# Kernel tuning notes

Hardware: AMD Instinct MI355X
Metric: run time of the kernel (lower is better)

The kernel has to match this reference:

```python
import jax, jax.numpy as jnp
import numpy as np
from jax import lax

B, N, NPOINT, NSAMPLE = 8, 8192, 2048, 32
RADIUS = 0.2
D_FEAT = 64
MLP = [64, 64, 128]
IN_CH = 3 + D_FEAT
EPS = 1e-5


def setup_inputs() -> dict:
    key = jax.random.key(0)
    ks = jax.random.split(key, 2 + len(MLP))
    inp = {
        "xyz": jax.random.uniform(ks[0], (B, N, 3), dtype=jnp.float32),
        "points": jax.random.normal(ks[1], (B, N, D_FEAT), dtype=jnp.float32),
    }
    cin = IN_CH
    for i, cout in enumerate(MLP):
        inp[f"W{i+1}"] = jax.random.normal(ks[2 + i], (cout, cin), dtype=jnp.float32) * 0.05
        inp[f"b{i+1}"] = jnp.zeros((cout,), jnp.float32)
        inp[f"g{i+1}"] = jnp.ones((cout,), jnp.float32)
        inp[f"be{i+1}"] = jnp.zeros((cout,), jnp.float32)
        cin = cout
    return inp


def farthest_point_sample(xyz, npoint):
    # xyz: (B, N, 3) -> (B, npoint) int32 indices. Deterministic start at index 0.
    Bb, Nn, _ = xyz.shape
    barange = jnp.arange(Bb)

    def step(carry, _):
        distance, farthest = carry
        centroid = xyz[barange, farthest]                      # (B, 3)
        d = jnp.sum((xyz - centroid[:, None, :]) ** 2, -1)     # (B, N)
        distance = jnp.minimum(distance, d)
        new_far = jnp.argmax(distance, axis=-1).astype(jnp.int32)
        return (distance, new_far), farthest

    init = (jnp.full((Bb, Nn), 1e10, xyz.dtype), jnp.zeros((Bb,), jnp.int32))
    _, idxs = lax.scan(step, init, None, length=npoint)        # (npoint, B)
    return idxs.T                                              # (B, npoint)


def index_points(points, idx):
    # points: (B, N, C); idx: (B, S) or (B, S, K)
    return jax.vmap(lambda p, i: p[i])(points, idx)


def square_distance(src, dst):
    # (B, S, C) x (B, N, C) -> (B, S, N)
    d = -2.0 * jnp.einsum('bsc,bnc->bsn', src, dst)
    d += jnp.sum(src ** 2, -1)[:, :, None]
    d += jnp.sum(dst ** 2, -1)[:, None, :]
    return d


def query_ball_point(radius, nsample, xyz, new_xyz):
    Bb, Nn, _ = xyz.shape
    sqr = square_distance(new_xyz, xyz)                        # (B, S, N)
    grid = jnp.arange(Nn, dtype=jnp.int32)
    group_idx = jnp.where(sqr > radius * radius, Nn, grid)     # invalid -> N
    # nsample smallest indices == torch sort(dim=-1)[:, :, :nsample]
    neg_vals, _ = lax.top_k(-group_idx, nsample)               # (B, S, K)
    group_idx = -neg_vals
    first = group_idx[:, :, 0:1]
    return jnp.where(group_idx == Nn, first, group_idx)


def bn_relu(x, gamma, beta):
    # x: (B, C, L). Training-mode batchnorm (biased variance) + ReLU.
    mean = jnp.mean(x, axis=(0, 2), keepdims=True)
    var = jnp.mean((x - mean) ** 2, axis=(0, 2), keepdims=True)
    xn = (x - mean) * lax.rsqrt(var + EPS)
    return jax.nn.relu(xn * gamma[None, :, None] + beta[None, :, None])


def reference(xyz, points, W1, b1, g1, be1, W2, b2, g2, be2, W3, b3, g3, be3):
    Bb = xyz.shape[0]
    fps_idx = farthest_point_sample(xyz, NPOINT)               # (B, S)
    new_xyz = index_points(xyz, fps_idx)                       # (B, S, 3)
    idx = query_ball_point(RADIUS, NSAMPLE, xyz, new_xyz)      # (B, S, K)
    grouped_xyz = index_points(xyz, idx)                       # (B, S, K, 3)
    grouped_xyz_norm = grouped_xyz - new_xyz[:, :, None, :]
    grouped_points = index_points(points, idx)                 # (B, S, K, D)
    g = jnp.concatenate([grouped_xyz_norm, grouped_points], -1)  # (B, S, K, C)
    x = g.reshape(Bb, NPOINT * NSAMPLE, -1).transpose(0, 2, 1)   # (B, C, S*K)
    for W, b, ga, be in ((W1, b1, g1, be1), (W2, b2, g2, be2), (W3, b3, g3, be3)):
        x = jnp.einsum('oc,bcl->bol', W, x) + b[None, :, None]
        x = bn_relu(x, ga, be)
    x = x.reshape(Bb, -1, NPOINT, NSAMPLE)
    new_points = jnp.max(x, axis=-1).transpose(0, 2, 1)        # (B, S, C_out)
    return new_xyz, new_points
```

## Files before the change

### kernel.cpp

```cpp
#include <hip/hip_runtime.h>
#include <hip/hip_bf16.h>

#define NB 8
#define NN 8192
#define NP 2048
#define NS 32
#define INV_P (1.0f/524288.0f)

typedef float v2f __attribute__((ext_vector_type(2)));

template<int CTRL>
__device__ __forceinline__ float fmax_dpp(float v) {
  const int x = __builtin_amdgcn_update_dpp(0, __float_as_int(v), CTRL, 0xF, 0xF, true);
  return fmaxf(v, __int_as_float(x));
}


__global__ __launch_bounds__(512)
void k_fps_pre(const float* __restrict__ xyz, const float* __restrict__ feat,
               const float* __restrict__ W1, const float* __restrict__ b1,
               float* __restrict__ F, float* __restrict__ outXyz, float* __restrict__ stats)
{
#pragma clang fp contract(off)
  __shared__ union U { float4 xyzw[NN]; float fx[128*64]; } sh;
  __shared__ unsigned long long cand[2][8];
  const int t = threadIdx.x;
  if (blockIdx.x < 8) {
    const int b = blockIdx.x;
    const float* xb = xyz + (size_t)b*NN*3;
    v2f px[8], py[8], pz[8], dd[8];
#pragma unroll
    for (int j = 0; j < 8; ++j) {
      const int i0 = t*16 + 2*j;
      const float x0 = xb[i0*3+0], y0 = xb[i0*3+1], z0 = xb[i0*3+2];
      const float x1 = xb[i0*3+3], y1 = xb[i0*3+4], z1 = xb[i0*3+5];
      px[j] = (v2f){x0,x1}; py[j] = (v2f){y0,y1}; pz[j] = (v2f){z0,z1};
      dd[j] = (v2f){1e10f,1e10f};
      sh.xyzw[i0]   = make_float4(x0,y0,z0,0.f);
      sh.xyzw[i0+1] = make_float4(x1,y1,z1,0.f);
    }
    __syncthreads();
    const int lane = t & 63, wv = t >> 6;
    float4 cf = sh.xyzw[0];
    for (int s = 0; s < NP; ++s) {
      if (t == 0) {
        float* o = outXyz + ((size_t)b*NP+s)*3;
        o[0]=cf.x; o[1]=cf.y; o[2]=cf.z;
      }
      const v2f cx = {cf.x,cf.x}, cy = {cf.y,cf.y}, cz = {cf.z,cf.z};
      float m = -1.f; int mi = 0;
#pragma unroll
      for (int j = 0; j < 8; ++j) {
        const v2f dx = px[j]-cx, dy = py[j]-cy, dz = pz[j]-cz;
        v2f d = dx*dx; d = d + dy*dy; d = d + dz*dz;
        const float n0 = fminf(dd[j].x, d.x);
        const float n1 = fminf(dd[j].y, d.y);
        dd[j].x = n0; dd[j].y = n1;
        if (n0 > m) { m = n0; mi = 2*j;   }
        if (n1 > m) { m = n1; mi = 2*j+1; }
      }
      float r = m;
      r = fmax_dpp<0xB1>(r);
      r = fmax_dpp<0x4E>(r);
      r = fmax_dpp<0x141>(r);
      r = fmax_dpp<0x140>(r);
      r = fmax_dpp<0x142>(r);
      r = fmax_dpp<0x143>(r);
      const int wmb  = __builtin_amdgcn_readlane(__float_as_int(r), 63);
      const float wm = __int_as_float(wmb);
      const unsigned long long mk = __ballot(m == wm);
      const int ls  = __ffsll((long long)mk) - 1;
      const int miw = __builtin_amdgcn_readlane(mi, ls);
      const unsigned idx = (unsigned)((wv*64 + ls)*16 + miw);
      if (lane == 0)
        cand[s&1][wv] = ((unsigned long long)(unsigned)wmb << 32)
                      | (unsigned long long)(0xFFFFFFFFu - idx);
      __syncthreads();
      unsigned long long best = cand[s&1][0];
#pragma unroll
      for (int w = 1; w < 8; ++w) { const unsigned long long c = cand[s&1][w]; if (c > best) best = c; }
      const int far = (int)(0xFFFFFFFFu - (unsigned)(best & 0xFFFFFFFFull));
      cf = sh.xyzw[far];
    }
  } else {
    if (blockIdx.x == 8) {
      for (int i = t; i < 512*16; i += 512) stats[i] = 0.f;
    }
    const int blk = blockIdx.x - 8;
    const int base = blk * 128;
    const int b = base >> 13;
    const int n0 = base & (NN-1);
    {
      const int row = t >> 2, seg = t & 3;
      const float* src = feat + ((size_t)(b*NN + n0 + row))*64 + seg*16;
#pragma unroll
      for (int k = 0; k < 4; ++k) {
        const float4 v = *(const float4*)(src + k*4);
        *(float4*)&sh.fx[row*64 + seg*16 + k*4] = v;
      }
    }
    __syncthreads();
    const int o = t & 63, wv = t >> 6;
    float w[64];
#pragma unroll
    for (int c = 0; c < 64; ++c) w[c] = W1[o*67 + 3 + c];
    const float bb = b1[o];
    for (int r = wv*16; r < wv*16+16; ++r) {
      float acc = bb;
#pragma unroll
      for (int c4 = 0; c4 < 16; ++c4) {
        const float4 xq = *(const float4*)&sh.fx[r*64 + c4*4];
        acc = fmaf(w[c4*4+0], xq.x, acc);
        acc = fmaf(w[c4*4+1], xq.y, acc);
        acc = fmaf(w[c4*4+2], xq.z, acc);
        acc = fmaf(w[c4*4+3], xq.w, acc);
      }
      F[((size_t)(b*NN + n0 + r))*64 + o] = acc;
    }
  }
}

__global__ __launch_bounds__(256)
void k_ball(const float* __restrict__ xyz, const float* __restrict__ newXyz,
            const float* __restrict__ F, const float* __restrict__ W1,
            __hip_bfloat16* __restrict__ y1, float* __restrict__ stats)
{
  __shared__ float xs[NN], ys[NN], zs[NN];
  __shared__ int sel[4][NS];
  const int t = threadIdx.x;
  const int b = blockIdx.x >> 5;
  const int chunk = blockIdx.x & 31;
  const float* xb = xyz + (size_t)b*NN*3;
  for (int i = t; i < NN; i += 256) {
    xs[i] = xb[i*3+0]; ys[i] = xb[i*3+1]; zs[i] = xb[i*3+2];
  }
  __syncthreads();
  const int lane = t & 63, wv = t >> 6;
  const float w0 = W1[lane*67+0], w1 = W1[lane*67+1], w2 = W1[lane*67+2];
  const double rr = 0.2*0.2;
  float ls = 0.f, lq = 0.f;
  for (int qi = 0; qi < 16; ++qi) {
    const int q  = chunk*64 + wv*16 + qi;
    const int gq = b*NP + q;
    const float cx = newXyz[(size_t)gq*3+0], cy = newXyz[(size_t)gq*3+1], cz = newXyz[(size_t)gq*3+2];
    const double cxd = (double)cx, cyd = (double)cy, czd = (double)cz;
    const double ssd = cxd*cxd + cyd*cyd + czd*czd;
    int have = 0;
    for (int c0 = 0; c0 < NN; c0 += 64) {
      const int i = c0 + lane;
      const double x = (double)xs[i], y = (double)ys[i], z = (double)zs[i];
      const double dot = x*cxd + y*cyd + z*czd;
      const double pn2 = x*x + y*y + z*z;
      const double d = -2.0*dot + ssd + pn2;
      const bool ok = d <= rr;
      const unsigned long long mk = __ballot(ok);
      const int rank = __popcll(mk & ((1ull<<lane)-1ull));
      if (ok && have + rank < NS) sel[wv][have+rank] = i;
      have += (int)__popcll(mk);
      if (have >= NS) break;
    }
    if (have > NS) have = NS;
    const int first = sel[wv][0];
    if (lane >= have && lane < NS) sel[wv][lane] = first;
    for (int j = 0; j < NS; ++j) {
      const int i = sel[wv][j];
      const float dxn = xs[i]-cx, dyn = ys[i]-cy, dzn = zs[i]-cz;
      const float f = F[((size_t)(b*NN+i))*64 + lane];
      float yv = fmaf(w0,dxn,f); yv = fmaf(w1,dyn,yv); yv = fmaf(w2,dzn,yv);
      y1[((size_t)gq*NS + j)*64 + lane] = __float2bfloat16(yv);
      ls += yv; lq = fmaf(yv,yv,lq);
    }
  }
  atomicAdd(&stats[(0 +lane)*16], ls);
  atomicAdd(&stats[(64+lane)*16], lq);
}

__device__ inline void stage_bn(const __hip_bfloat16* __restrict__ src, float* __restrict__ xt,
                                const float* __restrict__ A, const float* __restrict__ Bc,
                                int t, int blockBase)
{
  const uint4* s = (const uint4*)(src + ((size_t)(blockBase + t))*64);
  float* row = &xt[t*64];
  const int sw = t & 7;
#pragma unroll
  for (int g = 0; g < 8; ++g) {
    const uint4 v = s[g];
    const unsigned uu[4] = {v.x, v.y, v.z, v.w};
    const float4 Aq0 = ((const float4*)A)[g*2],  Aq1 = ((const float4*)A)[g*2+1];
    const float4 Bq0 = ((const float4*)Bc)[g*2], Bq1 = ((const float4*)Bc)[g*2+1];
    float e[8];
#pragma unroll
    for (int k = 0; k < 4; ++k) {
      const float f0 = __uint_as_float(uu[k] << 16);
      const float f1 = __uint_as_float(uu[k] & 0xFFFF0000u);
      const float a0 = (k<2) ? ((k==0)?Aq0.x:Aq0.z) : ((k==2)?Aq1.x:Aq1.z);
      const float a1 = (k<2) ? ((k==0)?Aq0.y:Aq0.w) : ((k==2)?Aq1.y:Aq1.w);
      const float bb0 = (k<2) ? ((k==0)?Bq0.x:Bq0.z) : ((k==2)?Bq1.x:Bq1.z);
      const float bb1 = (k<2) ? ((k==0)?Bq0.y:Bq0.w) : ((k==2)?Bq1.y:Bq1.w);
      e[k*2+0] = fmaxf(fmaf(f0, a0, bb0), 0.f);
      e[k*2+1] = fmaxf(fmaf(f1, a1, bb1), 0.f);
    }
    const float4 q0 = make_float4(e[0],e[1],e[2],e[3]);
    const float4 q1 = make_float4(e[4],e[5],e[6],e[7]);
    ((float4*)row)[(g*2)   ^ sw] = q0;
    ((float4*)row)[(g*2+1) ^ sw] = q1;
  }
}

__global__ __launch_bounds__(256)
void k_l2(const __hip_bfloat16* __restrict__ y1, float* __restrict__ stats,
          const float* __restrict__ g1, const float* __restrict__ be1,
          const float* __restrict__ W2, const float* __restrict__ b2,
          __hip_bfloat16* __restrict__ y2)
{
  __shared__ float xt[256*64];
  __shared__ float A[64], Bc[64], ssh[64], qsh[64];
  const int t = threadIdx.x;
  if (t < 64) {
    const float mean = stats[t*16] * INV_P;
    float var = stats[(64+t)*16] * INV_P - mean*mean;
    if (var < 0.f) var = 0.f;
    const float rs = rsqrtf(var + 1e-5f);
    const float a = rs * g1[t];
    A[t] = a; Bc[t] = fmaf(-mean, a, be1[t]);
    ssh[t] = 0.f; qsh[t] = 0.f;
  }
  const int lane = t & 63, wv = t >> 6;
  float w[64];
#pragma unroll
  for (int c4 = 0; c4 < 16; ++c4) {
    const float4 v = *(const float4*)(W2 + lane*64 + c4*4);
    w[c4*4+0]=v.x; w[c4*4+1]=v.y; w[c4*4+2]=v.z; w[c4*4+3]=v.w;
  }
  const float bo = b2[lane];
  __syncthreads();
  stage_bn(y1, xt, A, Bc, t, blockIdx.x*256);
  __syncthreads();
  float ls = 0.f, lq = 0.f;
  for (int pp = 0; pp < 64; ++pp) {
    const int p = wv*64 + pp;
    const int sw = p & 7;
    const float* row = &xt[p*64];
    float acc = bo;
#pragma unroll
    for (int c4 = 0; c4 < 16; ++c4) {
      const float4 xq = ((const float4*)row)[c4 ^ sw];
      acc = fmaf(w[c4*4+0], xq.x, acc);
      acc = fmaf(w[c4*4+1], xq.y, acc);
      acc = fmaf(w[c4*4+2], xq.z, acc);
      acc = fmaf(w[c4*4+3], xq.w, acc);
    }
    y2[((size_t)(blockIdx.x*256 + p))*64 + lane] = __float2bfloat16(acc);
    ls += acc; lq = fmaf(acc,acc,lq);
  }
  atomicAdd(&ssh[lane], ls);
  atomicAdd(&qsh[lane], lq);
  __syncthreads();
  if (t < 64) {
    atomicAdd(&stats[(128+t)*16], ssh[t]);
    atomicAdd(&stats[(192+t)*16], qsh[t]);
  }
}

__global__ __launch_bounds__(256)
void k_l3(const __hip_bfloat16* __restrict__ y2, float* __restrict__ stats,
          const float* __restrict__ g2, const float* __restrict__ be2,
          const float* __restrict__ W3, const float* __restrict__ b3,
          float* __restrict__ mxbuf, float* __restrict__ mnbuf)
{
  __shared__ float xt[256*64];
  __shared__ float A[64], Bc[64], ssh[128], qsh[128];
  const int t = threadIdx.x;
  if (t < 64) {
    const float mean = stats[(128+t)*16] * INV_P;
    float var = stats[(192+t)*16] * INV_P - mean*mean;
    if (var < 0.f) var = 0.f;
    const float rs = rsqrtf(var + 1e-5f);
    const float a = rs * g2[t];
    A[t] = a; Bc[t] = fmaf(-mean, a, be2[t]);
  }
  if (t < 128) { ssh[t]=0.f; qsh[t]=0.f; }
  const int lane = t & 63, wv = t >> 6;
  float w0[64], w1[64];
#pragma unroll
  for (int c4 = 0; c4 < 16; ++c4) {
    const float4 v  = *(const float4*)(W3 + lane*64 + c4*4);
    const float4 v2 = *(const float4*)(W3 + (size_t)(lane+64)*64 + c4*4);
    w0[c4*4+0]=v.x;  w0[c4*4+1]=v.y;  w0[c4*4+2]=v.z;  w0[c4*4+3]=v.w;
    w1[c4*4+0]=v2.x; w1[c4*4+1]=v2.y; w1[c4*4+2]=v2.z; w1[c4*4+3]=v2.w;
  }
  const float bo0 = b3[lane], bo1 = b3[lane+64];
  __syncthreads();
  stage_bn(y2, xt, A, Bc, t, blockIdx.x*256);
  __syncthreads();
  float ls0=0.f,lq0=0.f,ls1=0.f,lq1=0.f;
  for (int which = 0; which < 2; ++which) {
    float mx0 = -1e30f, mx1 = -1e30f, mn0 = 1e30f, mn1 = 1e30f;
    for (int j = 0; j < 32; ++j) {
      const int p = (wv*2+which)*32 + j;
      const int sw = p & 7;
      const float* row = &xt[p*64];
      float a0 = bo0, a1 = bo1;
#pragma unroll
      for (int c4 = 0; c4 < 16; ++c4) {
        const float4 xq = ((const float4*)row)[c4 ^ sw];
        a0 = fmaf(w0[c4*4+0], xq.x, a0); a0 = fmaf(w0[c4*4+1], xq.y, a0);
        a0 = fmaf(w0[c4*4+2], xq.z, a0); a0 = fmaf(w0[c4*4+3], xq.w, a0);
        a1 = fmaf(w1[c4*4+0], xq.x, a1); a1 = fmaf(w1[c4*4+1], xq.y, a1);
        a1 = fmaf(w1[c4*4+2], xq.z, a1); a1 = fmaf(w1[c4*4+3], xq.w, a1);
      }
      ls0 += a0; lq0 = fmaf(a0,a0,lq0);
      ls1 += a1; lq1 = fmaf(a1,a1,lq1);
      mx0 = fmaxf(mx0, a0); mn0 = fminf(mn0, a0);
      mx1 = fmaxf(mx1, a1); mn1 = fminf(mn1, a1);
    }
    const size_t gq = (size_t)blockIdx.x*8 + wv*2 + which;
    mxbuf[gq*128 + lane]      = mx0;  mnbuf[gq*128 + lane]      = mn0;
    mxbuf[gq*128 + 64 + lane] = mx1;  mnbuf[gq*128 + 64 + lane] = mn1;
  }
  atomicAdd(&ssh[lane], ls0);    atomicAdd(&qsh[lane], lq0);
  atomicAdd(&ssh[64+lane], ls1); atomicAdd(&qsh[64+lane], lq1);
  __syncthreads();
  if (t < 128) {
    atomicAdd(&stats[(256+t)*16], ssh[t]);
    atomicAdd(&stats[(384+t)*16], qsh[t]);
  }
}

__global__ __launch_bounds__(256)
void k_out2(const float* __restrict__ mxbuf, const float* __restrict__ mnbuf,
            const float* __restrict__ stats, const float* __restrict__ g3,
            const float* __restrict__ be3, float* __restrict__ out)
{
  const int idx = blockIdx.x*256 + threadIdx.x;
  const int ch = idx & 127;
  const float mean = stats[(256+ch)*16] * INV_P;
  float var = stats[(384+ch)*16] * INV_P - mean*mean;
  if (var < 0.f) var = 0.f;
  const float rs = rsqrtf(var + 1e-5f);
  const float a = rs * g3[ch];
  const float bc = fmaf(-mean, a, be3[ch]);
  const float x = (a >= 0.f) ? mxbuf[idx] : mnbuf[idx];
  out[49152 + idx] = fmaxf(fmaf(a, x, bc), 0.f);
}

extern "C" void kernel_launch(void* const* d_in, const int* in_sizes, int n_in,
                              void* d_out, int out_size, void* d_ws, size_t ws_size,
                              hipStream_t stream)
{
  const float* xyz = (const float*)d_in[0];
  const float* pts = (const float*)d_in[1];
  const float* W1  = (const float*)d_in[2];
  const float* b1  = (const float*)d_in[3];
  const float* g1  = (const float*)d_in[4];
  const float* be1 = (const float*)d_in[5];
  const float* W2  = (const float*)d_in[6];
  const float* b2_ = (const float*)d_in[7];
  const float* g2  = (const float*)d_in[8];
  const float* be2 = (const float*)d_in[9];
  const float* W3  = (const float*)d_in[10];
  const float* b3_ = (const float*)d_in[11];
  const float* g3  = (const float*)d_in[12];
  const float* be3 = (const float*)d_in[13];
  float* out = (float*)d_out;
  char* ws = (char*)d_ws;

  float* stats = (float*)(ws);
  float* F     = (float*)(ws + (1u<<20));
  float* mxbuf = (float*)(ws + (17u<<20));
  float* mnbuf = (float*)(ws + (25u<<20));
  __hip_bfloat16* y1 = (__hip_bfloat16*)(ws + (32u<<20));
  __hip_bfloat16* y2 = (__hip_bfloat16*)(ws + (112u<<20));

  k_fps_pre<<<520, 512, 0, stream>>>(xyz, pts, W1, b1, F, out, stats);
  k_ball<<<256, 256, 0, stream>>>(xyz, out, F, W1, y1, stats);
  k_l2<<<2048, 256, 0, stream>>>(y1, stats, g1, be1, W2, b2_, y2);
  k_l3<<<2048, 256, 0, stream>>>(y2, stats, g2, be2, W3, b3_, mxbuf, mnbuf);
  k_out2<<<8192, 256, 0, stream>>>(mxbuf, mnbuf, stats, g3, be3, out);
}
```

Before: 2.246 ms.

## Double threads per block in MLP layer kernels and interleave ball-query batches

Runs k_l2 and k_l3 with 512 threads per block instead of 256. Staging now uses two threads per row, and in k_l3 each wave computes one 64-channel half rather than both, which halves the weight registers per thread. k_ball's block index mapping is also changed so consecutive blocks cover different batches. The aim is more waves in flight and lower register pressure in the dense layers, at the cost of larger blocks and more LDS contention per CU.

```diff
diff --git a/kernel.cpp b/kernel.cpp
--- a/kernel.cpp
+++ b/kernel.cpp
@@ -128,8 +128,8 @@
   __shared__ float xs[NN], ys[NN], zs[NN];
   __shared__ int sel[4][NS];
   const int t = threadIdx.x;
-  const int b = blockIdx.x >> 5;
-  const int chunk = blockIdx.x & 31;
+  const int b = blockIdx.x & 7;
+  const int chunk = blockIdx.x >> 3;
   const float* xb = xyz + (size_t)b*NN*3;
   for (int i = t; i < NN; i += 256) {
     xs[i] = xb[i*3+0]; ys[i] = xb[i*3+1]; zs[i] = xb[i*3+2];
@@ -175,16 +175,18 @@
   atomicAdd(&stats[(64+lane)*16], lq);
 }
 
-__device__ inline void stage_bn(const __hip_bfloat16* __restrict__ src, float* __restrict__ xt,
-                                const float* __restrict__ A, const float* __restrict__ Bc,
-                                int t, int blockBase)
-{
-  const uint4* s = (const uint4*)(src + ((size_t)(blockBase + t))*64);
-  float* row = &xt[t*64];
-  const int sw = t & 7;
-#pragma unroll
-  for (int g = 0; g < 8; ++g) {
-    const uint4 v = s[g];
+__device__ inline void stage_bn512(const __hip_bfloat16* __restrict__ src, float* __restrict__ xt,
+                                   const float* __restrict__ A, const float* __restrict__ Bc,
+                                   int t, int blockBase)
+{
+  const int row = t >> 1, half = t & 1;
+  const uint4* s = (const uint4*)(src + ((size_t)(blockBase + row))*64 + half*32);
+  float* rowp = &xt[row*64];
+  const int sw = row & 7;
+#pragma unroll
+  for (int g0 = 0; g0 < 4; ++g0) {
+    const int g = half*4 + g0;
+    const uint4 v = s[g0];
     const unsigned uu[4] = {v.x, v.y, v.z, v.w};
     const float4 Aq0 = ((const float4*)A)[g*2],  Aq1 = ((const float4*)A)[g*2+1];
     const float4 Bq0 = ((const float4*)Bc)[g*2], Bq1 = ((const float4*)Bc)[g*2+1];
@@ -202,12 +204,12 @@
     }
     const float4 q0 = make_float4(e[0],e[1],e[2],e[3]);
     const float4 q1 = make_float4(e[4],e[5],e[6],e[7]);
-    ((float4*)row)[(g*2)   ^ sw] = q0;
-    ((float4*)row)[(g*2+1) ^ sw] = q1;
-  }
-}
-
-__global__ __launch_bounds__(256)
+    ((float4*)rowp)[(g*2)   ^ sw] = q0;
+    ((float4*)rowp)[(g*2+1) ^ sw] = q1;
+  }
+}
+
+__global__ __launch_bounds__(512)
 void k_l2(const __hip_bfloat16* __restrict__ y1, float* __restrict__ stats,
           const float* __restrict__ g1, const float* __restrict__ be1,
           const float* __restrict__ W2, const float* __restrict__ b2,
@@ -234,11 +236,11 @@
   }
   const float bo = b2[lane];
   __syncthreads();
-  stage_bn(y1, xt, A, Bc, t, blockIdx.x*256);
+  stage_bn512(y1, xt, A, Bc, t, blockIdx.x*256);
   __syncthreads();
   float ls = 0.f, lq = 0.f;
-  for (int pp = 0; pp < 64; ++pp) {
-    const int p = wv*64 + pp;
+  for (int pp = 0; pp < 32; ++pp) {
+    const int p = wv*32 + pp;
     const int sw = p & 7;
     const float* row = &xt[p*64];
     float acc = bo;
@@ -262,7 +264,7 @@
   }
 }
 
-__global__ __launch_bounds__(256)
+__global__ __launch_bounds__(512)
 void k_l3(const __hip_bfloat16* __restrict__ y2, float* __restrict__ stats,
           const float* __restrict__ g2, const float* __restrict__ be2,
           const float* __restrict__ W3, const float* __restrict__ b3,
@@ -281,45 +283,40 @@
   }
   if (t < 128) { ssh[t]=0.f; qsh[t]=0.f; }
   const int lane = t & 63, wv = t >> 6;
-  float w0[64], w1[64];
+  const int half = wv & 1, rquad = wv >> 1;
+  const int ch = half*64 + lane;
+  float w[64];
 #pragma unroll
   for (int c4 = 0; c4 < 16; ++c4) {
-    const float4 v  = *(const float4*)(W3 + lane*64 + c4*4);
-    const float4 v2 = *(const float4*)(W3 + (size_t)(lane+64)*64 + c4*4);
-    w0[c4*4+0]=v.x;  w0[c4*4+1]=v.y;  w0[c4*4+2]=v.z;  w0[c4*4+3]=v.w;
-    w1[c4*4+0]=v2.x; w1[c4*4+1]=v2.y; w1[c4*4+2]=v2.z; w1[c4*4+3]=v2.w;
-  }
-  const float bo0 = b3[lane], bo1 = b3[lane+64];
-  __syncthreads();
-  stage_bn(y2, xt, A, Bc, t, blockIdx.x*256);
-  __syncthreads();
-  float ls0=0.f,lq0=0.f,ls1=0.f,lq1=0.f;
+    const float4 v = *(const float4*)(W3 + (size_t)ch*64 + c4*4);
+    w[c4*4+0]=v.x; w[c4*4+1]=v.y; w[c4*4+2]=v.z; w[c4*4+3]=v.w;
+  }
+  const float bo = b3[ch];
+  __syncthreads();
+  stage_bn512(y2, xt, A, Bc, t, blockIdx.x*256);
+  __syncthreads();
+  float ls = 0.f, lq = 0.f;
   for (int which = 0; which < 2; ++which) {
-    float mx0 = -1e30f, mx1 = -1e30f, mn0 = 1e30f, mn1 = 1e30f;
+    float mx = -1e30f, mn = 1e30f;
     for (int j = 0; j < 32; ++j) {
-      const int p = (wv*2+which)*32 + j;
+      const int p = rquad*64 + which*32 + j;
       const int sw = p & 7;
       const float* row = &xt[p*64];
-      float a0 = bo0, a1 = bo1;
+      float a = bo;
 #pragma unroll
       for (int c4 = 0; c4 < 16; ++c4) {
         const float4 xq = ((const float4*)row)[c4 ^ sw];
-        a0 = fmaf(w0[c4*4+0], xq.x, a0); a0 = fmaf(w0[c4*4+1], xq.y, a0);
-        a0 = fmaf(w0[c4*4+2], xq.z, a0); a0 = fmaf(w0[c4*4+3], xq.w, a0);
-        a1 = fmaf(w1[c4*4+0], xq.x, a1); a1 = fmaf(w1[c4*4+1], xq.y, a1);
-        a1 = fmaf(w1[c4*4+2], xq.z, a1); a1 = fmaf(w1[c4*4+3], xq.w, a1);
-      }
-      ls0 += a0; lq0 = fmaf(a0,a0,lq0);
-      ls1 += a1; lq1 = fmaf(a1,a1,lq1);
-      mx0 = fmaxf(mx0, a0); mn0 = fminf(mn0, a0);
-      mx1 = fmaxf(mx1, a1); mn1 = fminf(mn1, a1);
-    }
-    const size_t gq = (size_t)blockIdx.x*8 + wv*2 + which;
-    mxbuf[gq*128 + lane]      = mx0;  mnbuf[gq*128 + lane]      = mn0;
-    mxbuf[gq*128 + 64 + lane] = mx1;  mnbuf[gq*128 + 64 + lane] = mn1;
-  }
-  atomicAdd(&ssh[lane], ls0);    atomicAdd(&qsh[lane], lq0);
-  atomicAdd(&ssh[64+lane], ls1); atomicAdd(&qsh[64+lane], lq1);
+        a = fmaf(w[c4*4+0], xq.x, a); a = fmaf(w[c4*4+1], xq.y, a);
+        a = fmaf(w[c4*4+2], xq.z, a); a = fmaf(w[c4*4+3], xq.w, a);
+      }
+      ls += a; lq = fmaf(a,a,lq);
+      mx = fmaxf(mx, a); mn = fminf(mn, a);
+    }
+    const size_t gq = (size_t)blockIdx.x*8 + rquad*2 + which;
+    mxbuf[gq*128 + ch] = mx;  mnbuf[gq*128 + ch] = mn;
+  }
+  atomicAdd(&ssh[ch], ls);
+  atomicAdd(&qsh[ch], lq);
   __syncthreads();
   if (t < 128) {
     atomicAdd(&stats[(256+t)*16], ssh[t]);
@@ -374,7 +371,7 @@
 
   k_fps_pre<<<520, 512, 0, stream>>>(xyz, pts, W1, b1, F, out, stats);
   k_ball<<<256, 256, 0, stream>>>(xyz, out, F, W1, y1, stats);
-  k_l2<<<2048, 256, 0, stream>>>(y1, stats, g1, be1, W2, b2_, y2);
-  k_l3<<<2048, 256, 0, stream>>>(y2, stats, g2, be2, W3, b3_, mxbuf, mnbuf);
+  k_l2<<<2048, 512, 0, stream>>>(y1, stats, g1, be1, W2, b2_, y2);
+  k_l3<<<2048, 512, 0, stream>>>(y2, stats, g2, be2, W3, b3_, mxbuf, mnbuf);
   k_out2<<<8192, 256, 0, stream>>>(mxbuf, mnbuf, stats, g3, be3, out);
 }
```

Result: no change. 2.262 ms (+0.7%).
